# Kernel tuning notes

Measured on AMD Instinct MI355X. Metric: run time of the kernel, lower is better.

## Reference

```python
import jax, jax.numpy as jnp
import numpy as np

THRESHOLD = 0.7


def ternary_dequant(w, threshold=THRESHOLD):
    """Ternary quantize {-1,0,+1} with masked-mean alpha, return ternary*alpha."""
    abs_w = jnp.abs(w)
    delta = threshold * jnp.mean(abs_w)
    ternary = jnp.where(w > delta, 1.0, jnp.where(w < -delta, -1.0, 0.0)).astype(w.dtype)
    nz = ternary != 0
    cnt = jnp.sum(nz)
    # alpha = mean(|w| over nonzero ternary entries); fall back to mean(|w|) if all-zero
    masked_sum = jnp.sum(jnp.where(nz, abs_w, 0.0))
    alpha = jnp.where(cnt > 0, masked_sum / jnp.maximum(cnt, 1).astype(w.dtype), jnp.mean(abs_w))
    return ternary * alpha


def setup_inputs() -> dict:
    key = jax.random.key(0)
    kx, kw, kb = jax.random.split(key, 3)
    B, S, D_IN, D_OUT = 4, 2048, 4096, 4096
    x = jax.random.normal(kx, (B * S, D_IN), dtype=jnp.float32)
    # xavier-uniform-ish init for latent FP32 weights
    limit = np.sqrt(6.0 / (D_IN + D_OUT)).astype(np.float32)
    weight = jax.random.uniform(kw, (D_OUT, D_IN), dtype=jnp.float32, minval=-limit, maxval=limit)
    bias = jax.random.normal(kb, (D_OUT,), dtype=jnp.float32) * 0.02
    return {"x": x, "weight": weight, "bias": bias}


def reference(x, weight, bias):
    q_weight = ternary_dequant(weight)  # (out, in)
    return jnp.matmul(x, q_weight.T) + bias  # (tokens, out)
```

## Files before the change

kernel.cpp:

```cpp
#include <hip/hip_runtime.h>

#define M_DIM 8192
#define N_DIM 4096
#define K_DIM 4096

typedef __attribute__((ext_vector_type(8))) __bf16 bf16x8;
typedef __attribute__((ext_vector_type(4))) __bf16 bf16x4;
typedef __attribute__((ext_vector_type(4))) float floatx4;

__device__ __forceinline__ void async_copy16(const void* g, void* l) {
    __builtin_amdgcn_global_load_lds(
        (const __attribute__((address_space(1))) void*)g,
        (__attribute__((address_space(3))) void*)l,
        16, 0, 0);
}

__device__ __forceinline__ double wave_reduce_d(double v) {
    #pragma unroll
    for (int o = 32; o > 0; o >>= 1) v += __shfl_down(v, o, 64);
    return v;
}
__device__ __forceinline__ unsigned wave_reduce_u(unsigned v) {
    #pragma unroll
    for (int o = 32; o > 0; o >>= 1) v += __shfl_down(v, o, 64);
    return v;
}

__global__ __launch_bounds__(256) void k_pre(const float4* __restrict__ w4,
                                             double* __restrict__ part,
                                             const float4* __restrict__ x4,
                                             bf16x4* __restrict__ xb) {
    const int tid = threadIdx.x;
    if (blockIdx.x < 2048) {
        int idx = blockIdx.x * 256 + tid;
        double s = 0.0;
        #pragma unroll
        for (int it = 0; it < 8; ++it) {
            float4 v = w4[idx + it * (2048 * 256)];
            s += (double)fabsf(v.x) + (double)fabsf(v.y) +
                 (double)fabsf(v.z) + (double)fabsf(v.w);
        }
        s = wave_reduce_d(s);
        __shared__ double sm[4];
        if ((tid & 63) == 0) sm[tid >> 6] = s;
        __syncthreads();
        if (tid == 0) part[blockIdx.x] = sm[0] + sm[1] + sm[2] + sm[3];
    } else {
        int idx = (blockIdx.x - 2048) * 256 + tid;
        #pragma unroll
        for (int it = 0; it < 4; ++it) {
            int i = idx + it * (8192 * 256);
            float4 v = x4[i];
            bf16x4 o;
            o[0] = (__bf16)v.x; o[1] = (__bf16)v.y;
            o[2] = (__bf16)v.z; o[3] = (__bf16)v.w;
            xb[i] = o;
        }
    }
}

__global__ __launch_bounds__(256) void k_quant(const float4* __restrict__ w4,
                                               bf16x4* __restrict__ tern,
                                               const double* __restrict__ part,
                                               double* __restrict__ scal,
                                               double* __restrict__ pm,
                                               unsigned* __restrict__ pc) {
    const int tid = threadIdx.x;
    double s = 0.0;
    #pragma unroll
    for (int i = 0; i < 8; ++i) s += part[tid + i * 256];
    s = wave_reduce_d(s);
    __shared__ double sm[4];
    if ((tid & 63) == 0) sm[tid >> 6] = s;
    __syncthreads();
    const double mean = (sm[0] + sm[1] + sm[2] + sm[3]) * (1.0 / 16777216.0);
    const double delta = 0.7 * mean;
    if (blockIdx.x == 0 && tid == 0) scal[0] = mean;

    int idx = blockIdx.x * 256 + tid;
    double msum = 0.0;
    unsigned cnt = 0;
    #pragma unroll
    for (int it = 0; it < 8; ++it) {
        int i = idx + it * (2048 * 256);
        float4 v = w4[i];
        float e[4] = {v.x, v.y, v.z, v.w};
        bf16x4 o;
        #pragma unroll
        for (int c = 0; c < 4; ++c) {
            float wv = e[c];
            float t = ((double)wv > delta) ? 1.0f
                    : (((double)wv < -delta) ? -1.0f : 0.0f);
            if (t != 0.0f) { msum += (double)fabsf(wv); cnt++; }
            o[c] = (__bf16)t;
        }
        tern[i] = o;
    }
    msum = wave_reduce_d(msum);
    cnt  = wave_reduce_u(cnt);
    __shared__ double smd[4];
    __shared__ unsigned smu[4];
    if ((tid & 63) == 0) { smd[tid >> 6] = msum; smu[tid >> 6] = cnt; }
    __syncthreads();
    if (tid == 0) {
        pm[blockIdx.x] = smd[0] + smd[1] + smd[2] + smd[3];
        pc[blockIdx.x] = smu[0] + smu[1] + smu[2] + smu[3];
    }
}

__global__ __launch_bounds__(256, 2) void ternary_gemm(
    const __bf16* __restrict__ A,
    const __bf16* __restrict__ B,
    const float*  __restrict__ bias,
    const double* __restrict__ scal,
    const double* __restrict__ pm,
    const unsigned* __restrict__ pc,
    float* __restrict__ C)
{
    __shared__ __attribute__((aligned(128))) __bf16 As[256 * 32];
    __shared__ __attribute__((aligned(128))) __bf16 Bs[128 * 32];
    __shared__ double smd[4];
    __shared__ unsigned smu[4];

    const int tid  = threadIdx.x;
    const int wave = tid >> 6;
    const int lane = tid & 63;
    const int quad = lane >> 4;
    const int l16  = lane & 15;
    const int wr = wave >> 1;
    const int wc = wave & 1;

    const int br = blockIdx.y;
    const int bc = blockIdx.x;

    const int srow = lane >> 2;
    const int scol = ((lane & 3) ^ ((srow >> 1) & 3)) * 8;

    const __bf16* gA[4];
    const __bf16* gB[2];
    __bf16* lA[4];
    __bf16* lB[2];
    #pragma unroll
    for (int t = 0; t < 4; ++t) {
        const int c = wave * 4 + t;
        gA[t] = A + (size_t)(br * 256 + c * 16 + srow) * K_DIM + scol;
        lA[t] = &As[c * 512];
    }
    #pragma unroll
    for (int t = 0; t < 2; ++t) {
        const int c = wave * 2 + t;
        gB[t] = B + (size_t)(bc * 128 + c * 16 + srow) * K_DIM + scol;
        lB[t] = &Bs[c * 512];
    }

    floatx4 acc[8][4] = {};

    const int swz = (quad ^ ((l16 >> 1) & 3)) * 8;
    const int a_off = (wr * 128 + l16) * 32 + swz;
    const int b_off = (wc * 64 + l16) * 32 + swz;

    for (int k0 = 0; k0 < K_DIM; k0 += 32) {
        #pragma unroll
        for (int t = 0; t < 4; ++t) { async_copy16(gA[t], lA[t]); gA[t] += 32; }
        #pragma unroll
        for (int t = 0; t < 2; ++t) { async_copy16(gB[t], lB[t]); gB[t] += 32; }
        __syncthreads();

        bf16x8 af[8], bfr[4];
        #pragma unroll
        for (int i = 0; i < 8; ++i)
            af[i] = *(const bf16x8*)&As[a_off + i * 512];
        #pragma unroll
        for (int j = 0; j < 4; ++j)
            bfr[j] = *(const bf16x8*)&Bs[b_off + j * 512];

        #pragma unroll
        for (int i = 0; i < 8; ++i)
            #pragma unroll
            for (int j = 0; j < 4; ++j)
                acc[i][j] = __builtin_amdgcn_mfma_f32_16x16x32_bf16(
                    af[i], bfr[j], acc[i][j], 0, 0, 0);
        __syncthreads();
    }

    double s = 0.0; unsigned c = 0;
    #pragma unroll
    for (int i = 0; i < 8; ++i) { s += pm[tid + i * 256]; c += pc[tid + i * 256]; }
    s = wave_reduce_d(s);
    c = wave_reduce_u(c);
    if ((tid & 63) == 0) { smd[tid >> 6] = s; smu[tid >> 6] = c; }
    __syncthreads();
    const double ms = smd[0] + smd[1] + smd[2] + smd[3];
    const unsigned ct = smu[0] + smu[1] + smu[2] + smu[3];
    const float alpha = (float)(ct > 0 ? ms / (double)ct : scal[0]);

    float bv[4];
    #pragma unroll
    for (int j = 0; j < 4; ++j)
        bv[j] = bias[bc * 128 + wc * 64 + j * 16 + l16];

    #pragma unroll
    for (int i = 0; i < 8; ++i) {
        const int row0 = br * 256 + wr * 128 + i * 16 + quad * 4;
        #pragma unroll
        for (int j = 0; j < 4; ++j) {
            const int col = bc * 128 + wc * 64 + j * 16 + l16;
            #pragma unroll
            for (int r = 0; r < 4; ++r)
                C[(size_t)(row0 + r) * N_DIM + col] = acc[i][j][r] * alpha + bv[j];
        }
    }
}

extern "C" void kernel_launch(void* const* d_in, const int* in_sizes, int n_in,
                              void* d_out, int out_size, void* d_ws, size_t ws_size,
                              hipStream_t stream) {
    const float* x    = (const float*)d_in[0];
    const float* w    = (const float*)d_in[1];
    const float* bias = (const float*)d_in[2];
    float* out = (float*)d_out;

    char* ws = (char*)d_ws;
    double*   d_scal = (double*)ws;
    double*   part   = (double*)(ws + 64);
    double*   pm     = (double*)(ws + 16448);
    unsigned* pc     = (unsigned*)(ws + 32832);
    __bf16*   xb     = (__bf16*)(ws + 65536);
    __bf16*   tern   = (__bf16*)(ws + 65536 + (size_t)M_DIM * K_DIM * 2);

    k_pre<<<10240, 256, 0, stream>>>((const float4*)w, part, (const float4*)x, (bf16x4*)xb);
    k_quant<<<2048, 256, 0, stream>>>((const float4*)w, (bf16x4*)tern, part, d_scal, pm, pc);

    dim3 grid(N_DIM / 128, M_DIM / 256);
    ternary_gemm<<<grid, 256, 0, stream>>>(xb, tern, bias, d_scal, pm, pc, out);
}
```

Baseline: 554.9 us.

## Enlarge GEMM tile to 256x256 with 4-stage async LDS pipeline

The GEMM now uses 512-thread blocks computing 256x256 output tiles, in place of 256-thread blocks computing 256x128 tiles. A four-buffer LDS ring is filled by async global-to-LDS loads issued three k-steps ahead, with explicit vmcnt waits and split A/B staging interleaved with MFMA phases under raised priority. Blocks are remapped across XCDs for locality. This targets the per-iteration load latency and the double barrier of the old single-buffer loop, and raises operand reuse, at the cost of 64KB of LDS, more register pressure, and fragile hand-placed barrier and waitcnt logic.

```diff
diff --git a/kernel.cpp b/kernel.cpp
--- a/kernel.cpp
+++ b/kernel.cpp
@@ -13,6 +13,12 @@
         (const __attribute__((address_space(1))) void*)g,
         (__attribute__((address_space(3))) void*)l,
         16, 0, 0);
+}
+
+__device__ __forceinline__ void block_sync() {
+    asm volatile("" ::: "memory");
+    __builtin_amdgcn_s_barrier();
+    asm volatile("" ::: "memory");
 }
 
 __device__ __forceinline__ double wave_reduce_d(double v) {
@@ -108,7 +114,7 @@
     }
 }
 
-__global__ __launch_bounds__(256, 2) void ternary_gemm(
+__global__ __launch_bounds__(512, 2) void ternary_gemm(
     const __bf16* __restrict__ A,
     const __bf16* __restrict__ B,
     const float*  __restrict__ bias,
@@ -117,94 +123,127 @@
     const unsigned* __restrict__ pc,
     float* __restrict__ C)
 {
-    __shared__ __attribute__((aligned(128))) __bf16 As[256 * 32];
-    __shared__ __attribute__((aligned(128))) __bf16 Bs[128 * 32];
-    __shared__ double smd[4];
-    __shared__ unsigned smu[4];
+    __shared__ __attribute__((aligned(128))) __bf16 As[4][8192];
+    __shared__ __attribute__((aligned(128))) __bf16 Bs[4][8192];
+    __shared__ double smd[8];
+    __shared__ unsigned smu[8];
 
     const int tid  = threadIdx.x;
-    const int wave = tid >> 6;
+    const int w    = tid >> 6;
     const int lane = tid & 63;
     const int quad = lane >> 4;
     const int l16  = lane & 15;
-    const int wr = wave >> 1;
-    const int wc = wave & 1;
-
-    const int br = blockIdx.y;
-    const int bc = blockIdx.x;
+    const int wr = w >> 2;
+    const int wc = w & 3;
+
+    const int id = (blockIdx.x & 7) * 64 + (blockIdx.x >> 3);
+    const int br = id >> 4;
+    const int bc = id & 15;
 
     const int srow = lane >> 2;
     const int scol = ((lane & 3) ^ ((srow >> 1) & 3)) * 8;
 
-    const __bf16* gA[4];
-    const __bf16* gB[2];
-    __bf16* lA[4];
-    __bf16* lB[2];
-    #pragma unroll
-    for (int t = 0; t < 4; ++t) {
-        const int c = wave * 4 + t;
-        gA[t] = A + (size_t)(br * 256 + c * 16 + srow) * K_DIM + scol;
-        lA[t] = &As[c * 512];
-    }
-    #pragma unroll
-    for (int t = 0; t < 2; ++t) {
-        const int c = wave * 2 + t;
-        gB[t] = B + (size_t)(bc * 128 + c * 16 + srow) * K_DIM + scol;
-        lB[t] = &Bs[c * 512];
-    }
+    const __bf16* gA0 = A + (size_t)(br * 256 + w * 16 + srow) * K_DIM + scol;
+    const __bf16* gA1 = gA0 + (size_t)128 * K_DIM;
+    const __bf16* gB0 = B + (size_t)(bc * 256 + w * 16 + srow) * K_DIM + scol;
+    const __bf16* gB1 = gB0 + (size_t)128 * K_DIM;
 
     floatx4 acc[8][4] = {};
 
-    const int swz = (quad ^ ((l16 >> 1) & 3)) * 8;
+    const int swz   = (quad ^ ((l16 >> 1) & 3)) * 8;
     const int a_off = (wr * 128 + l16) * 32 + swz;
     const int b_off = (wc * 64 + l16) * 32 + swz;
 
-    for (int k0 = 0; k0 < K_DIM; k0 += 32) {
-        #pragma unroll
-        for (int t = 0; t < 4; ++t) { async_copy16(gA[t], lA[t]); gA[t] += 32; }
-        #pragma unroll
-        for (int t = 0; t < 2; ++t) { async_copy16(gB[t], lB[t]); gB[t] += 32; }
-        __syncthreads();
-
-        bf16x8 af[8], bfr[4];
-        #pragma unroll
-        for (int i = 0; i < 8; ++i)
-            af[i] = *(const bf16x8*)&As[a_off + i * 512];
-        #pragma unroll
-        for (int j = 0; j < 4; ++j)
-            bfr[j] = *(const bf16x8*)&Bs[b_off + j * 512];
-
-        #pragma unroll
-        for (int i = 0; i < 8; ++i)
-            #pragma unroll
-            for (int j = 0; j < 4; ++j)
-                acc[i][j] = __builtin_amdgcn_mfma_f32_16x16x32_bf16(
-                    af[i], bfr[j], acc[i][j], 0, 0, 0);
-        __syncthreads();
-    }
+#define STAGE_A(ktt) do {                                        \
+        const int _sb = (ktt) & 3; const int _so = (ktt) * 32;   \
+        async_copy16(gA0 + _so, &As[_sb][w * 512]);              \
+        async_copy16(gA1 + _so, &As[_sb][(w + 8) * 512]);        \
+    } while (0)
+#define STAGE_B(ktt) do {                                        \
+        const int _sb = (ktt) & 3; const int _so = (ktt) * 32;   \
+        async_copy16(gB0 + _so, &Bs[_sb][w * 512]);              \
+        async_copy16(gB1 + _so, &Bs[_sb][(w + 8) * 512]);        \
+    } while (0)
+
+    STAGE_A(0); STAGE_B(0);
+    STAGE_A(1); STAGE_B(1);
+    STAGE_A(2); STAGE_B(2);
+
+#define TILE(kt_, VMN, DO_STAGE_) do {                                         \
+        asm volatile("s_waitcnt vmcnt(" #VMN ")" ::: "memory");                \
+        block_sync();                                                          \
+        const int _buf = (kt_) & 3;                                            \
+        const __bf16* _Ab = As[_buf];                                          \
+        const __bf16* _Bb = Bs[_buf];                                          \
+        bf16x8 _a[4], _b[4];                                                   \
+        _Pragma("unroll")                                                      \
+        for (int i = 0; i < 4; ++i)                                            \
+            _a[i] = *(const bf16x8*)(_Ab + a_off + i * 512);                   \
+        _Pragma("unroll")                                                      \
+        for (int j = 0; j < 4; ++j)                                            \
+            _b[j] = *(const bf16x8*)(_Bb + b_off + j * 512);                   \
+        if (DO_STAGE_) STAGE_A((kt_) + 3);                                     \
+        block_sync();                                                          \
+        __builtin_amdgcn_sched_barrier(0);                                     \
+        __builtin_amdgcn_s_setprio(1);                                         \
+        _Pragma("unroll")                                                      \
+        for (int i = 0; i < 4; ++i)                                            \
+            _Pragma("unroll")                                                  \
+            for (int j = 0; j < 4; ++j)                                        \
+                acc[i][j] = __builtin_amdgcn_mfma_f32_16x16x32_bf16(           \
+                    _a[i], _b[j], acc[i][j], 0, 0, 0);                         \
+        __builtin_amdgcn_s_setprio(0);                                         \
+        __builtin_amdgcn_sched_barrier(0);                                     \
+        block_sync();                                                          \
+        _Pragma("unroll")                                                      \
+        for (int i = 0; i < 4; ++i)                                            \
+            _a[i] = *(const bf16x8*)(_Ab + a_off + (4 + i) * 512);             \
+        if (DO_STAGE_) STAGE_B((kt_) + 3);                                     \
+        block_sync();                                                          \
+        __builtin_amdgcn_sched_barrier(0);                                     \
+        __builtin_amdgcn_s_setprio(1);                                         \
+        _Pragma("unroll")                                                      \
+        for (int i = 0; i < 4; ++i)                                            \
+            _Pragma("unroll")                                                  \
+            for (int j = 0; j < 4; ++j)                                        \
+                acc[4 + i][j] = __builtin_amdgcn_mfma_f32_16x16x32_bf16(       \
+                    _a[i], _b[j], acc[4 + i][j], 0, 0, 0);                     \
+        __builtin_amdgcn_s_setprio(0);                                         \
+        __builtin_amdgcn_sched_barrier(0);                                     \
+    } while (0)
+
+    for (int kt = 0; kt < 125; ++kt) TILE(kt, 8, true);
+    TILE(125, 8, false);
+    TILE(126, 4, false);
+    TILE(127, 0, false);
+
+#undef TILE
+#undef STAGE_A
+#undef STAGE_B
 
     double s = 0.0; unsigned c = 0;
     #pragma unroll
-    for (int i = 0; i < 8; ++i) { s += pm[tid + i * 256]; c += pc[tid + i * 256]; }
+    for (int i = 0; i < 4; ++i) { s += pm[tid + i * 512]; c += pc[tid + i * 512]; }
     s = wave_reduce_d(s);
     c = wave_reduce_u(c);
-    if ((tid & 63) == 0) { smd[tid >> 6] = s; smu[tid >> 6] = c; }
+    if (lane == 0) { smd[w] = s; smu[w] = c; }
     __syncthreads();
-    const double ms = smd[0] + smd[1] + smd[2] + smd[3];
-    const unsigned ct = smu[0] + smu[1] + smu[2] + smu[3];
+    double ms = 0.0; unsigned ct = 0;
+    #pragma unroll
+    for (int i = 0; i < 8; ++i) { ms += smd[i]; ct += smu[i]; }
     const float alpha = (float)(ct > 0 ? ms / (double)ct : scal[0]);
 
     float bv[4];
     #pragma unroll
     for (int j = 0; j < 4; ++j)
-        bv[j] = bias[bc * 128 + wc * 64 + j * 16 + l16];
+        bv[j] = bias[bc * 256 + wc * 64 + j * 16 + l16];
 
     #pragma unroll
     for (int i = 0; i < 8; ++i) {
         const int row0 = br * 256 + wr * 128 + i * 16 + quad * 4;
         #pragma unroll
         for (int j = 0; j < 4; ++j) {
-            const int col = bc * 128 + wc * 64 + j * 16 + l16;
+            const int col = bc * 256 + wc * 64 + j * 16 + l16;
             #pragma unroll
             for (int r = 0; r < 4; ++r)
                 C[(size_t)(row0 + r) * N_DIM + col] = acc[i][j][r] * alpha + bv[j];
@@ -231,6 +270,5 @@
     k_pre<<<10240, 256, 0, stream>>>((const float4*)w, part, (const float4*)x, (bf16x4*)xb);
     k_quant<<<2048, 256, 0, stream>>>((const float4*)w, (bf16x4*)tern, part, d_scal, pm, pc);
 
-    dim3 grid(N_DIM / 128, M_DIM / 256);
-    ternary_gemm<<<grid, 256, 0, stream>>>(xb, tern, bias, d_scal, pm, pc, out);
-}
+    ternary_gemm<<<512, 512, 0, stream>>>(xb, tern, bias, d_scal, pm, pc, out);
+}
```

After: 602.3 us. +8.6%, slower.
